# Kernel optimization log

Measured on AMD Instinct MI355X. Metric: run time of the kernel, lower is better.

The kernel has to match this reference:

```python
import jax, jax.numpy as jnp
import numpy as np
import math

B, S, D, H, E = 4, 4096, 256, 8, 262144
HD = D // H
ITER_NUM = 4
TEMP = 1.0
LN_EPS = 1e-12
N = B * S


def setup_inputs() -> dict:
    key = jax.random.key(0)
    ks = jax.random.split(key, 6)
    return {
        "hidden_states": jax.random.normal(ks[0], (B, S, D), dtype=jnp.float32),
        "attention_mask": jnp.zeros((B, S), dtype=jnp.float32),
        "src": jax.random.randint(ks[1], (E,), 0, N),
        "dst": jax.random.randint(ks[2], (E,), 0, N),
        "Wqkv": jax.random.normal(ks[3], (D, 3 * D), dtype=jnp.float32) * 0.02,
        "bqkv": jnp.zeros((3 * D,), dtype=jnp.float32),
        "Wo": jax.random.normal(ks[4], (D, D), dtype=jnp.float32) * 0.02,
        "bo": jnp.zeros((D,), dtype=jnp.float32),
        "gamma": jnp.ones((D,), dtype=jnp.float32),
        "beta": jnp.zeros((D,), dtype=jnp.float32),
    }


def _gn_attn(hidden_states, attention_mask, src, dst, Wqkv, bqkv, Wo, bo, gamma, beta):
    # qkv projection (node ordering is batch-major: node = b*S + s)
    qkv = hidden_states @ Wqkv + bqkv                      # [B,S,3D]
    q, k, v = jnp.split(qkv, 3, axis=-1)
    q = q / math.sqrt(HD)
    qn = q.reshape(N, H, HD)
    kn = k.reshape(N, H, HD)
    vn = v.reshape(N, H, HD)
    node_mask = (attention_mask >= 0).reshape(N)           # [N] bool

    # per-edge dot-product scores: u_dot_v('k','q') -> dot(k[src], q[dst])
    score = jnp.einsum("ehd,ehd->eh", kn[src], qn[dst])    # [E,H]
    edge_mask = node_mask[src] & node_mask[dst]
    score = jnp.where(edge_mask[:, None], score, jnp.float32(-10000.0))

    # edge softmax over incoming edges of each dst node (per head)
    mx = jax.ops.segment_max(score, dst, num_segments=N)   # [N,H]
    es = jnp.exp(score - mx[dst])
    den = jax.ops.segment_sum(es, dst, num_segments=N)     # [N,H]
    attn = es / den[dst]                                   # [E,H]

    # diffusion (heat-kernel / PPR-style) message passing
    h = math.exp(-TEMP) * vn                               # [N,H,HD]
    gather = h
    fact = 1.0
    for ki in range(1, ITER_NUM):
        msg = attn[:, :, None] * h[src]                    # [E,H,HD]
        h = jax.ops.segment_sum(msg, dst, num_segments=N)  # [N,H,HD]
        fact = fact * (TEMP / ki)
        gather = gather + fact * h

    attn_out = gather.reshape(B, S, D)

    # output projection + residual + LayerNorm
    y = attn_out @ Wo + bo + hidden_states
    mu = jnp.mean(y, axis=-1, keepdims=True)
    var = jnp.mean(jnp.square(y - mu), axis=-1, keepdims=True)
    return (y - mu) / jnp.sqrt(var + LN_EPS) * gamma + beta


def reference(hidden_states, attention_mask, src, dst, Wqkv, bqkv, Wo, bo, gamma, beta):
    return _gn_attn(hidden_states, attention_mask, src, dst, Wqkv, bqkv, Wo, bo, gamma, beta)
```

## Files before the change

kernel.cpp:

```cpp
#include <hip/hip_runtime.h>
#include <math.h>

#define NN 16384
#define DD 256
#define HH 8
#define EE 262144
#define D3 768
#define QSCALE 0.17677669529663687f
#define EXPN1 0.36787944117144233f
#define LN_EPS 1e-12f

typedef short bf16x8 __attribute__((ext_vector_type(8)));
typedef float f32x4 __attribute__((ext_vector_type(4)));
typedef float f32x2 __attribute__((ext_vector_type(2)));
typedef unsigned short u16;
typedef unsigned char u8;

__device__ __forceinline__ float bf_lo(unsigned u) { return __uint_as_float(u << 16); }
__device__ __forceinline__ float bf_hi(unsigned u) { return __uint_as_float(u & 0xffff0000u); }
__device__ __forceinline__ unsigned f2bf(float f) {
    unsigned b = __float_as_uint(f);
    return (b + 0x7fffu + ((b >> 16) & 1u)) >> 16;
}
__device__ __forceinline__ unsigned pack2bf(float lo, float hi) {
    return f2bf(lo) | (f2bf(hi) << 16);
}
__device__ __forceinline__ u8 f2fp8(float v) {
    return (u8)(__builtin_amdgcn_cvt_pk_fp8_f32(v, v, 0, false) & 0xff);
}

__global__ void prep_kernel(const float* __restrict__ hidden, unsigned* __restrict__ hidb,
                            const float* __restrict__ Wqkv, const float* __restrict__ bqkv,
                            u16* __restrict__ WtQ, float* __restrict__ biasq,
                            const float* __restrict__ Wo, const float* __restrict__ bo,
                            u16* __restrict__ WtO, float* __restrict__ biaso,
                            const int* __restrict__ dst, int* __restrict__ deg) {
    int b = blockIdx.x;
    if (b < 4096) {
        int gid = b * 256 + threadIdx.x;
        float4 v = *(const float4*)(hidden + (size_t)gid * 4);
        *(uint2*)(hidb + (size_t)gid * 2) = make_uint2(pack2bf(v.x, v.y), pack2bf(v.z, v.w));
    } else if (b < 4864) {
        int gid = (b - 4096) * 256 + threadIdx.x;
        int n = gid >> 8, k = gid & 255;
        float s = (n < DD) ? QSCALE : 1.0f;
        WtQ[(size_t)n * 256 + k] = (u16)f2bf(Wqkv[(size_t)k * D3 + n] * s);
        if (k == 0) biasq[n] = bqkv[n] * s;
    } else if (b < 5120) {
        int gid = (b - 4864) * 256 + threadIdx.x;
        int n = gid >> 8, k = gid & 255;
        WtO[(size_t)n * 256 + k] = (u16)f2bf(Wo[(size_t)k * DD + n]);
        if (k == 0) biaso[n] = bo[n];
    } else {
        int e = (b - 5120) * 256 + threadIdx.x;
        atomicAdd(&deg[dst[e]], 1);
    }
}

__global__ __launch_bounds__(256) void mfma_gemm1_kernel(
        const u16* __restrict__ Ab, const u16* __restrict__ Bt,
        const float* __restrict__ bias,
        u16* __restrict__ qb, u8* __restrict__ kb8,
        u8* __restrict__ h8, u16* __restrict__ gb) {
    __shared__ u16 As[128 * 40];
    __shared__ u16 Bs[128 * 40];
    const int tid = threadIdx.x;
    const int m0 = blockIdx.y * 128;
    const int n0 = blockIdx.x * 128;
    const int wave = tid >> 6, lane = tid & 63;
    const int wr = wave >> 1, wc = wave & 1;
    const int lm = lane & 15, quad = lane >> 4;

    f32x4 acc[4][4] = {};
    const int r0 = tid >> 2;
    const int c8 = (tid & 3) * 8;

    for (int k0 = 0; k0 < 256; k0 += 32) {
        #pragma unroll
        for (int s = 0; s < 2; ++s) {
            int r = r0 + s * 64;
            *(uint4*)&As[r * 40 + c8] = *(const uint4*)(Ab + (size_t)(m0 + r) * 256 + k0 + c8);
            *(uint4*)&Bs[r * 40 + c8] = *(const uint4*)(Bt + (size_t)(n0 + r) * 256 + k0 + c8);
        }
        __syncthreads();
        bf16x8 af[4], bfv[4];
        #pragma unroll
        for (int mi = 0; mi < 4; ++mi)
            af[mi] = *(const bf16x8*)&As[(wr * 64 + mi * 16 + lm) * 40 + quad * 8];
        #pragma unroll
        for (int ni = 0; ni < 4; ++ni)
            bfv[ni] = *(const bf16x8*)&Bs[(wc * 64 + ni * 16 + lm) * 40 + quad * 8];
        #pragma unroll
        for (int mi = 0; mi < 4; ++mi)
            #pragma unroll
            for (int ni = 0; ni < 4; ++ni)
                acc[mi][ni] = __builtin_amdgcn_mfma_f32_16x16x32_bf16(
                    af[mi], bfv[ni], acc[mi][ni], 0, 0, 0);
        __syncthreads();
    }

    const int type = n0 >> 8;
    const int cb = n0 & 255;
    #pragma unroll
    for (int mi = 0; mi < 4; ++mi) {
        #pragma unroll
        for (int j = 0; j < 4; ++j) {
            int m = m0 + wr * 64 + mi * 16 + quad * 4 + j;
            #pragma unroll
            for (int ni = 0; ni < 4; ++ni) {
                int nl = wc * 64 + ni * 16 + lm;
                float val = acc[mi][ni][j] + bias[n0 + nl];
                size_t off = (size_t)m * 256 + cb + nl;
                if (type == 0) qb[off] = (u16)f2bf(val);
                else if (type == 1) kb8[off] = f2fp8(val);
                else {
                    float hx = val * EXPN1;
                    h8[off] = f2fp8(hx);
                    gb[off] = (u16)f2bf(hx);
                }
            }
        }
    }
}

__global__ __launch_bounds__(1024) void scan_kernel(const int* __restrict__ deg,
                                                    int* __restrict__ offs,
                                                    int* __restrict__ cursor, int n) {
    __shared__ int part[1024];
    int t = threadIdx.x;
    int base = t * 16;
    int local[16];
    int s = 0;
    #pragma unroll
    for (int i = 0; i < 16; ++i) { local[i] = s; s += deg[base + i]; }
    part[t] = s;
    __syncthreads();
    for (int d = 1; d < 1024; d <<= 1) {
        int add = (t >= d) ? part[t - d] : 0;
        __syncthreads();
        part[t] += add;
        __syncthreads();
    }
    int excl = part[t] - s;
    #pragma unroll
    for (int i = 0; i < 16; ++i) {
        offs[base + i] = excl + local[i];
        cursor[base + i] = excl + local[i];
    }
    if (t == 1023) offs[n] = excl + s;
}

__global__ void scatter_kernel(const int* __restrict__ src, const int* __restrict__ dst,
                               int* __restrict__ cursor, int* __restrict__ srcs) {
    int e = blockIdx.x * 256 + threadIdx.x;
    int pos = atomicAdd(&cursor[dst[e]], 1);
    srcs[pos] = src[e];
}

__device__ __forceinline__ float edge_score(const unsigned qq[16], const u8* __restrict__ kb8,
                                            const float* __restrict__ amask,
                                            int s, int h, bool dvalid) {
    const uint4* kp = (const uint4*)(kb8 + (size_t)s * 256 + h * 32);
    uint4 k0 = kp[0], k1 = kp[1];
    unsigned kk[8] = {k0.x, k0.y, k0.z, k0.w, k1.x, k1.y, k1.z, k1.w};
    float acc = 0.0f;
    #pragma unroll
    for (int t = 0; t < 8; ++t) {
        f32x2 a = __builtin_amdgcn_cvt_pk_f32_fp8(kk[t], false);
        f32x2 b = __builtin_amdgcn_cvt_pk_f32_fp8(kk[t], true);
        acc += a.x * bf_lo(qq[2 * t]) + a.y * bf_hi(qq[2 * t]);
        acc += b.x * bf_lo(qq[2 * t + 1]) + b.y * bf_hi(qq[2 * t + 1]);
    }
    bool valid = dvalid && (amask[s] >= 0.0f);
    return valid ? acc : -10000.0f;
}

__global__ __launch_bounds__(256) void edge_softmax_kernel(
        const unsigned* __restrict__ qb, const u8* __restrict__ kb8,
        const int* __restrict__ offs, const int* __restrict__ srcs,
        const float* __restrict__ amask, float* __restrict__ attn) {
    const int wave = threadIdx.x >> 6, lane = threadIdx.x & 63;
    const int node = blockIdx.x * 4 + wave;
    const int h = lane & 7;
    const int eo = lane >> 3;
    const int beg = offs[node], end = offs[node + 1];
    const int cnt = end - beg;
    const uint4* qp = (const uint4*)(qb + (size_t)node * 128 + h * 16);
    uint4 q0 = qp[0], q1 = qp[1], q2 = qp[2], q3 = qp[3];
    unsigned qq[16] = {q0.x, q0.y, q0.z, q0.w, q1.x, q1.y, q1.z, q1.w,
                       q2.x, q2.y, q2.z, q2.w, q3.x, q3.y, q3.z, q3.w};
    const bool dvalid = amask[node] >= 0.0f;

    if (cnt <= 64) {
        float esb[8];
        float m = -1e30f;
        #pragma unroll
        for (int it = 0; it < 8; ++it) {
            int i = beg + it * 8 + eo;
            float sc = -1e30f;
            if (i < end) sc = edge_score(qq, kb8, amask, srcs[i], h, dvalid);
            esb[it] = sc;
            m = fmaxf(m, sc);
        }
        m = fmaxf(m, __shfl_xor(m, 8));
        m = fmaxf(m, __shfl_xor(m, 16));
        m = fmaxf(m, __shfl_xor(m, 32));
        float den = 0.0f;
        #pragma unroll
        for (int it = 0; it < 8; ++it) {
            int i = beg + it * 8 + eo;
            if (i < end) { float es = __expf(esb[it] - m); esb[it] = es; den += es; }
        }
        den += __shfl_xor(den, 8);
        den += __shfl_xor(den, 16);
        den += __shfl_xor(den, 32);
        float iv = (cnt > 0) ? 1.0f / den : 0.0f;
        #pragma unroll
        for (int it = 0; it < 8; ++it) {
            int i = beg + it * 8 + eo;
            if (i < end) attn[(size_t)i * 8 + h] = esb[it] * iv;
        }
    } else {
        float m = -1e30f;
        for (int i0 = beg; i0 < end; i0 += 8) {
            int i = i0 + eo;
            if (i < end) {
                float sc = edge_score(qq, kb8, amask, srcs[i], h, dvalid);
                attn[(size_t)i * 8 + h] = sc;
                m = fmaxf(m, sc);
            }
        }
        m = fmaxf(m, __shfl_xor(m, 8));
        m = fmaxf(m, __shfl_xor(m, 16));
        m = fmaxf(m, __shfl_xor(m, 32));
        float den = 0.0f;
        for (int i0 = beg; i0 < end; i0 += 8) {
            int i = i0 + eo;
            if (i < end) {
                float es = __expf(attn[(size_t)i * 8 + h] - m);
                attn[(size_t)i * 8 + h] = es;
                den += es;
            }
        }
        den += __shfl_xor(den, 8);
        den += __shfl_xor(den, 16);
        den += __shfl_xor(den, 32);
        float iv = 1.0f / den;
        for (int i0 = beg; i0 < end; i0 += 8) {
            int i = i0 + eo;
            if (i < end) attn[(size_t)i * 8 + h] *= iv;
        }
    }
}

__global__ void diffuse_kernel(const int* __restrict__ offs, const int* __restrict__ srcs,
                               const float* __restrict__ attn,
                               const unsigned* __restrict__ hcur, unsigned* __restrict__ hnext,
                               uint2* __restrict__ gb, float fact) {
    int gid = blockIdx.x * 256 + threadIdx.x;
    int node = gid >> 6;
    int j2 = gid & 63;
    int h = j2 >> 3;
    int beg = offs[node], end = offs[node + 1];
    float a0 = 0.0f, a1 = 0.0f, a2 = 0.0f, a3 = 0.0f;
    int i = beg;
    for (; i + 8 <= end; i += 8) {
        int sarr[8]; float aarr[8]; unsigned hv[8];
        #pragma unroll
        for (int t = 0; t < 8; ++t) {
            sarr[t] = srcs[i + t];
            aarr[t] = attn[(size_t)(i + t) * 8 + h];
        }
        #pragma unroll
        for (int t = 0; t < 8; ++t) hv[t] = hcur[(size_t)sarr[t] * 64 + j2];
        #pragma unroll
        for (int t = 0; t < 8; ++t) {
            float a = aarr[t];
            f32x2 lo = __builtin_amdgcn_cvt_pk_f32_fp8(hv[t], false);
            f32x2 hi = __builtin_amdgcn_cvt_pk_f32_fp8(hv[t], true);
            a0 += a * lo.x; a1 += a * lo.y;
            a2 += a * hi.x; a3 += a * hi.y;
        }
    }
    if (i < end) {
        int cnt = end - i;
        int sarr[8]; float aarr[8]; unsigned hv[8];
        #pragma unroll
        for (int t = 0; t < 8; ++t) if (t < cnt) {
            sarr[t] = srcs[i + t];
            aarr[t] = attn[(size_t)(i + t) * 8 + h];
        }
        #pragma unroll
        for (int t = 0; t < 8; ++t) if (t < cnt) hv[t] = hcur[(size_t)sarr[t] * 64 + j2];
        #pragma unroll
        for (int t = 0; t < 8; ++t) if (t < cnt) {
            float a = aarr[t];
            f32x2 lo = __builtin_amdgcn_cvt_pk_f32_fp8(hv[t], false);
            f32x2 hi = __builtin_amdgcn_cvt_pk_f32_fp8(hv[t], true);
            a0 += a * lo.x; a1 += a * lo.y;
            a2 += a * hi.x; a3 += a * hi.y;
        }
    }
    if (hnext) {
        int pk = __builtin_amdgcn_cvt_pk_fp8_f32(a0, a1, 0, false);
        pk = __builtin_amdgcn_cvt_pk_fp8_f32(a2, a3, pk, true);
        hnext[(size_t)node * 64 + j2] = (unsigned)pk;
    }
    uint2* gp = gb + (size_t)node * 64 + j2;
    uint2 g = *gp;
    float g0 = bf_lo(g.x) + fact * a0;
    float g1 = bf_hi(g.x) + fact * a1;
    float g2 = bf_lo(g.y) + fact * a2;
    float g3 = bf_hi(g.y) + fact * a3;
    *gp = make_uint2(pack2bf(g0, g1), pack2bf(g2, g3));
}

__global__ __launch_bounds__(256) void gemm2_ln_kernel(
        const u16* __restrict__ Ab, const u16* __restrict__ Bt,
        const float* __restrict__ bias, const float* __restrict__ resid,
        const float* __restrict__ gamma, const float* __restrict__ beta,
        float* __restrict__ out) {
    __shared__ u16 As[64 * 40];
    __shared__ u16 Bs[256 * 40];
    const int tid = threadIdx.x;
    const int m0 = blockIdx.x * 64;
    const int wave = tid >> 6, lane = tid & 63;
    const int lm = lane & 15, quad = lane >> 4;

    f32x4 acc[16] = {};
    for (int k0 = 0; k0 < 256; k0 += 32) {
        *(uint4*)&As[(tid >> 2) * 40 + (tid & 3) * 8] =
            *(const uint4*)(Ab + (size_t)(m0 + (tid >> 2)) * 256 + k0 + (tid & 3) * 8);
        {
            const uint4* srcp = (const uint4*)(Bt + (size_t)tid * 256 + k0);
            uint4* dstp = (uint4*)&Bs[tid * 40];
            dstp[0] = srcp[0]; dstp[1] = srcp[1]; dstp[2] = srcp[2]; dstp[3] = srcp[3];
        }
        __syncthreads();
        bf16x8 af = *(const bf16x8*)&As[(wave * 16 + lm) * 40 + quad * 8];
        #pragma unroll
        for (int ni = 0; ni < 16; ++ni) {
            bf16x8 bfv = *(const bf16x8*)&Bs[(ni * 16 + lm) * 40 + quad * 8];
            acc[ni] = __builtin_amdgcn_mfma_f32_16x16x32_bf16(af, bfv, acc[ni], 0, 0, 0);
        }
        __syncthreads();
    }

    const int mrow = m0 + wave * 16 + quad * 4;
    float ga[16], be[16];
    float rowsum[4] = {}, rowsq[4] = {};
    #pragma unroll
    for (int ni = 0; ni < 16; ++ni) {
        int col = ni * 16 + lm;
        float bia = bias[col];
        ga[ni] = gamma[col]; be[ni] = beta[col];
        #pragma unroll
        for (int j = 0; j < 4; ++j) {
            float val = acc[ni][j] + bia + resid[(size_t)(mrow + j) * 256 + col];
            acc[ni][j] = val;
            rowsum[j] += val;
            rowsq[j] += val * val;
        }
    }
    #pragma unroll
    for (int j = 0; j < 4; ++j) {
        #pragma unroll
        for (int msk = 1; msk <= 8; msk <<= 1) {
            rowsum[j] += __shfl_xor(rowsum[j], msk);
            rowsq[j] += __shfl_xor(rowsq[j], msk);
        }
    }
    float mu[4], rstd[4];
    #pragma unroll
    for (int j = 0; j < 4; ++j) {
        mu[j] = rowsum[j] * (1.0f / 256.0f);
        float var = rowsq[j] * (1.0f / 256.0f) - mu[j] * mu[j];
        rstd[j] = 1.0f / sqrtf(var + LN_EPS);
    }
    #pragma unroll
    for (int ni = 0; ni < 16; ++ni) {
        int col = ni * 16 + lm;
        #pragma unroll
        for (int j = 0; j < 4; ++j)
            out[(size_t)(mrow + j) * 256 + col] = (acc[ni][j] - mu[j]) * rstd[j] * ga[ni] + be[ni];
    }
}

extern "C" void kernel_launch(void* const* d_in, const int* in_sizes, int n_in,
                              void* d_out, int out_size, void* d_ws, size_t ws_size,
                              hipStream_t stream) {
    const float* hidden = (const float*)d_in[0];
    const float* amask  = (const float*)d_in[1];
    const int*   src    = (const int*)d_in[2];
    const int*   dst    = (const int*)d_in[3];
    const float* Wqkv   = (const float*)d_in[4];
    const float* bqkv   = (const float*)d_in[5];
    const float* Wo     = (const float*)d_in[6];
    const float* bo     = (const float*)d_in[7];
    const float* gamma  = (const float*)d_in[8];
    const float* beta   = (const float*)d_in[9];
    float* out = (float*)d_out;

    char* p = (char*)d_ws;
    u16*      hidb   = (u16*)p;      p += (size_t)NN * DD * 2;
    u16*      WtQ    = (u16*)p;      p += (size_t)D3 * DD * 2;
    u16*      WtO    = (u16*)p;      p += (size_t)DD * DD * 2;
    float*    biasq  = (float*)p;    p += (size_t)D3 * 4;
    float*    biaso  = (float*)p;    p += (size_t)DD * 4;
    u16*      qb     = (u16*)p;      p += (size_t)NN * DD * 2;
    u8*       kb8    = (u8*)p;       p += (size_t)NN * DD;
    u8*       h8A    = (u8*)p;       p += (size_t)NN * DD;
    u8*       h8B    = (u8*)p;       p += (size_t)NN * DD;
    u16*      gb     = (u16*)p;      p += (size_t)NN * DD * 2;
    float*    attn   = (float*)p;    p += (size_t)EE * HH * 4;
    int*      deg    = (int*)p;      p += (size_t)NN * 4;
    int*      offs   = (int*)p;      p += (size_t)(NN + 1) * 4;
    int*      cursor = (int*)p;      p += (size_t)NN * 4;
    int*      srcs   = (int*)p;      p += (size_t)EE * 4;

    hipMemsetAsync(deg, 0, (size_t)NN * 4, stream);
    prep_kernel<<<6144, 256, 0, stream>>>(hidden, (unsigned*)hidb,
                                          Wqkv, bqkv, WtQ, biasq,
                                          Wo, bo, WtO, biaso, dst, deg);

    scan_kernel<<<1, 1024, 0, stream>>>(deg, offs, cursor, NN);
    scatter_kernel<<<EE / 256, 256, 0, stream>>>(src, dst, cursor, srcs);

    mfma_gemm1_kernel<<<dim3(D3 / 128, NN / 128), 256, 0, stream>>>(
        hidb, WtQ, biasq, qb, kb8, h8A, gb);

    edge_softmax_kernel<<<NN / 4, 256, 0, stream>>>(
        (const unsigned*)qb, kb8, offs, srcs, amask, attn);

    diffuse_kernel<<<(NN * 64) / 256, 256, 0, stream>>>(
        offs, srcs, attn, (const unsigned*)h8A, (unsigned*)h8B, (uint2*)gb, 1.0f);
    diffuse_kernel<<<(NN * 64) / 256, 256, 0, stream>>>(
        offs, srcs, attn, (const unsigned*)h8B, (unsigned*)h8A, (uint2*)gb, 0.5f);
    diffuse_kernel<<<(NN * 64) / 256, 256, 0, stream>>>(
        offs, srcs, attn, (const unsigned*)h8A, nullptr, (uint2*)gb, 1.0f / 6.0f);

    gemm2_ln_kernel<<<NN / 64, 256, 0, stream>>>(
        gb, WtO, biaso, hidden, gamma, beta, out);
}
```

Before: 222.8 us.

## Fuse scatter into GEMM1 launch and first diffusion into edge softmax

```diff
diff --git a/kernel.cpp b/kernel.cpp
--- a/kernel.cpp
+++ b/kernel.cpp
@@ -57,16 +57,52 @@
     }
 }
 
-__global__ __launch_bounds__(256) void mfma_gemm1_kernel(
+__global__ __launch_bounds__(1024) void scan_kernel(const int* __restrict__ deg,
+                                                    int* __restrict__ offs,
+                                                    int* __restrict__ cursor, int n) {
+    __shared__ int part[1024];
+    int t = threadIdx.x;
+    int base = t * 16;
+    int local[16];
+    int s = 0;
+    #pragma unroll
+    for (int i = 0; i < 16; ++i) { local[i] = s; s += deg[base + i]; }
+    part[t] = s;
+    __syncthreads();
+    for (int d = 1; d < 1024; d <<= 1) {
+        int add = (t >= d) ? part[t - d] : 0;
+        __syncthreads();
+        part[t] += add;
+        __syncthreads();
+    }
+    int excl = part[t] - s;
+    #pragma unroll
+    for (int i = 0; i < 16; ++i) {
+        offs[base + i] = excl + local[i];
+        cursor[base + i] = excl + local[i];
+    }
+    if (t == 1023) offs[n] = excl + s;
+}
+
+__global__ __launch_bounds__(256) void gemm1_scatter_kernel(
         const u16* __restrict__ Ab, const u16* __restrict__ Bt,
         const float* __restrict__ bias,
         u16* __restrict__ qb, u8* __restrict__ kb8,
-        u8* __restrict__ h8, u16* __restrict__ gb) {
+        u8* __restrict__ h8, u16* __restrict__ gb,
+        const int* __restrict__ src, const int* __restrict__ dst,
+        int* __restrict__ cursor, int* __restrict__ srcs) {
     __shared__ u16 As[128 * 40];
     __shared__ u16 Bs[128 * 40];
+    if (blockIdx.x < 1024) {
+        int e = blockIdx.x * 256 + threadIdx.x;
+        int pos = atomicAdd(&cursor[dst[e]], 1);
+        srcs[pos] = src[e];
+        return;
+    }
+    const int bid = blockIdx.x - 1024;
     const int tid = threadIdx.x;
-    const int m0 = blockIdx.y * 128;
-    const int n0 = blockIdx.x * 128;
+    const int m0 = (bid / 6) * 128;
+    const int n0 = (bid % 6) * 128;
     const int wave = tid >> 6, lane = tid & 63;
     const int wr = wave >> 1, wc = wave & 1;
     const int lm = lane & 15, quad = lane >> 4;
@@ -123,40 +159,6 @@
     }
 }
 
-__global__ __launch_bounds__(1024) void scan_kernel(const int* __restrict__ deg,
-                                                    int* __restrict__ offs,
-                                                    int* __restrict__ cursor, int n) {
-    __shared__ int part[1024];
-    int t = threadIdx.x;
-    int base = t * 16;
-    int local[16];
-    int s = 0;
-    #pragma unroll
-    for (int i = 0; i < 16; ++i) { local[i] = s; s += deg[base + i]; }
-    part[t] = s;
-    __syncthreads();
-    for (int d = 1; d < 1024; d <<= 1) {
-        int add = (t >= d) ? part[t - d] : 0;
-        __syncthreads();
-        part[t] += add;
-        __syncthreads();
-    }
-    int excl = part[t] - s;
-    #pragma unroll
-    for (int i = 0; i < 16; ++i) {
-        offs[base + i] = excl + local[i];
-        cursor[base + i] = excl + local[i];
-    }
-    if (t == 1023) offs[n] = excl + s;
-}
-
-__global__ void scatter_kernel(const int* __restrict__ src, const int* __restrict__ dst,
-                               int* __restrict__ cursor, int* __restrict__ srcs) {
-    int e = blockIdx.x * 256 + threadIdx.x;
-    int pos = atomicAdd(&cursor[dst[e]], 1);
-    srcs[pos] = src[e];
-}
-
 __device__ __forceinline__ float edge_score(const unsigned qq[16], const u8* __restrict__ kb8,
                                             const float* __restrict__ amask,
                                             int s, int h, bool dvalid) {
@@ -175,30 +177,44 @@
     return valid ? acc : -10000.0f;
 }
 
-__global__ __launch_bounds__(256) void edge_softmax_kernel(
+__global__ __launch_bounds__(256) void softmax_diffuse1_kernel(
         const unsigned* __restrict__ qb, const u8* __restrict__ kb8,
         const int* __restrict__ offs, const int* __restrict__ srcs,
-        const float* __restrict__ amask, float* __restrict__ attn) {
+        const float* __restrict__ amask, float* __restrict__ attn,
+        const unsigned* __restrict__ hA, unsigned* __restrict__ hB,
+        uint2* __restrict__ gb) {
+    __shared__ int   s_src[4][64];
+    __shared__ float s_att[4][512];
     const int wave = threadIdx.x >> 6, lane = threadIdx.x & 63;
     const int node = blockIdx.x * 4 + wave;
     const int h = lane & 7;
     const int eo = lane >> 3;
     const int beg = offs[node], end = offs[node + 1];
     const int cnt = end - beg;
+    const int j2 = lane;
+    uint2 g = gb[(size_t)node * 64 + j2];
+
     const uint4* qp = (const uint4*)(qb + (size_t)node * 128 + h * 16);
     uint4 q0 = qp[0], q1 = qp[1], q2 = qp[2], q3 = qp[3];
     unsigned qq[16] = {q0.x, q0.y, q0.z, q0.w, q1.x, q1.y, q1.z, q1.w,
                        q2.x, q2.y, q2.z, q2.w, q3.x, q3.y, q3.z, q3.w};
     const bool dvalid = amask[node] >= 0.0f;
-
-    if (cnt <= 64) {
+    const bool fast = (cnt <= 64);
+
+    if (fast) {
+        int sarr[8];
+        #pragma unroll
+        for (int it = 0; it < 8; ++it) {
+            int i = beg + it * 8 + eo;
+            sarr[it] = (i < end) ? srcs[i] : 0;
+        }
         float esb[8];
         float m = -1e30f;
         #pragma unroll
         for (int it = 0; it < 8; ++it) {
             int i = beg + it * 8 + eo;
             float sc = -1e30f;
-            if (i < end) sc = edge_score(qq, kb8, amask, srcs[i], h, dvalid);
+            if (i < end) sc = edge_score(qq, kb8, amask, sarr[it], h, dvalid);
             esb[it] = sc;
             m = fmaxf(m, sc);
         }
@@ -218,7 +234,12 @@
         #pragma unroll
         for (int it = 0; it < 8; ++it) {
             int i = beg + it * 8 + eo;
-            if (i < end) attn[(size_t)i * 8 + h] = esb[it] * iv;
+            if (i < end) {
+                float a = esb[it] * iv;
+                attn[(size_t)i * 8 + h] = a;
+                s_att[wave][(it * 8 + eo) * 8 + h] = a;
+                if (h == 0) s_src[wave][it * 8 + eo] = sarr[it];
+            }
         }
     } else {
         float m = -1e30f;
@@ -251,6 +272,62 @@
             if (i < end) attn[(size_t)i * 8 + h] *= iv;
         }
     }
+    __syncthreads();
+
+    const int hh = j2 >> 3;
+    float a0 = 0.0f, a1 = 0.0f, a2 = 0.0f, a3 = 0.0f;
+    if (fast) {
+        for (int e0 = 0; e0 < cnt; e0 += 8) {
+            int sa[8]; float aa[8]; unsigned hv[8];
+            #pragma unroll
+            for (int t = 0; t < 8; ++t) {
+                bool ok = (e0 + t < cnt);
+                sa[t] = ok ? s_src[wave][e0 + t] : 0;
+                aa[t] = ok ? s_att[wave][(e0 + t) * 8 + hh] : 0.0f;
+            }
+            #pragma unroll
+            for (int t = 0; t < 8; ++t)
+                hv[t] = (e0 + t < cnt) ? hA[(size_t)sa[t] * 64 + j2] : 0u;
+            #pragma unroll
+            for (int t = 0; t < 8; ++t) {
+                float a = aa[t];
+                f32x2 lo = __builtin_amdgcn_cvt_pk_f32_fp8(hv[t], false);
+                f32x2 hi = __builtin_amdgcn_cvt_pk_f32_fp8(hv[t], true);
+                a0 += a * lo.x; a1 += a * lo.y;
+                a2 += a * hi.x; a3 += a * hi.y;
+            }
+        }
+    } else {
+        for (int i0 = beg; i0 < end; i0 += 8) {
+            int lim = end - i0;
+            int sa[8]; float aa[8]; unsigned hv[8];
+            #pragma unroll
+            for (int t = 0; t < 8; ++t) {
+                bool ok = (t < lim);
+                sa[t] = ok ? srcs[i0 + t] : 0;
+                aa[t] = ok ? attn[(size_t)(i0 + t) * 8 + hh] : 0.0f;
+            }
+            #pragma unroll
+            for (int t = 0; t < 8; ++t)
+                hv[t] = (t < lim) ? hA[(size_t)sa[t] * 64 + j2] : 0u;
+            #pragma unroll
+            for (int t = 0; t < 8; ++t) {
+                float a = aa[t];
+                f32x2 lo = __builtin_amdgcn_cvt_pk_f32_fp8(hv[t], false);
+                f32x2 hi = __builtin_amdgcn_cvt_pk_f32_fp8(hv[t], true);
+                a0 += a * lo.x; a1 += a * lo.y;
+                a2 += a * hi.x; a3 += a * hi.y;
+            }
+        }
+    }
+    int pk = __builtin_amdgcn_cvt_pk_fp8_f32(a0, a1, 0, false);
+    pk = __builtin_amdgcn_cvt_pk_fp8_f32(a2, a3, pk, true);
+    hB[(size_t)node * 64 + j2] = (unsigned)pk;
+    float g0 = bf_lo(g.x) + a0;
+    float g1 = bf_hi(g.x) + a1;
+    float g2 = bf_lo(g.y) + a2;
+    float g3 = bf_hi(g.y) + a3;
+    gb[(size_t)node * 64 + j2] = make_uint2(pack2bf(g0, g1), pack2bf(g2, g3));
 }
 
 __global__ void diffuse_kernel(const int* __restrict__ offs, const int* __restrict__ srcs,
@@ -262,17 +339,30 @@
     int j2 = gid & 63;
     int h = j2 >> 3;
     int beg = offs[node], end = offs[node + 1];
+    uint2* gp = gb + (size_t)node * 64 + j2;
+    uint2 g = *gp;
     float a0 = 0.0f, a1 = 0.0f, a2 = 0.0f, a3 = 0.0f;
-    int i = beg;
-    for (; i + 8 <= end; i += 8) {
-        int sarr[8]; float aarr[8]; unsigned hv[8];
+    int nfull = (end - beg) >> 3;
+    int sarr[8]; float aarr[8];
+    if (nfull > 0) {
         #pragma unroll
         for (int t = 0; t < 8; ++t) {
-            sarr[t] = srcs[i + t];
-            aarr[t] = attn[(size_t)(i + t) * 8 + h];
-        }
+            sarr[t] = srcs[beg + t];
+            aarr[t] = attn[(size_t)(beg + t) * 8 + h];
+        }
+    }
+    for (int c = 0; c < nfull; ++c) {
+        unsigned hv[8];
         #pragma unroll
         for (int t = 0; t < 8; ++t) hv[t] = hcur[(size_t)sarr[t] * 64 + j2];
+        int sn[8]; float an[8];
+        bool more = (c + 1 < nfull);
+        int nb = beg + (c + 1) * 8;
+        #pragma unroll
+        for (int t = 0; t < 8; ++t) {
+            sn[t] = more ? srcs[nb + t] : 0;
+            an[t] = more ? attn[(size_t)(nb + t) * 8 + h] : 0.0f;
+        }
         #pragma unroll
         for (int t = 0; t < 8; ++t) {
             float a = aarr[t];
@@ -281,20 +371,25 @@
             a0 += a * lo.x; a1 += a * lo.y;
             a2 += a * hi.x; a3 += a * hi.y;
         }
-    }
+        #pragma unroll
+        for (int t = 0; t < 8; ++t) { sarr[t] = sn[t]; aarr[t] = an[t]; }
+    }
+    int i = beg + nfull * 8;
     if (i < end) {
-        int cnt = end - i;
-        int sarr[8]; float aarr[8]; unsigned hv[8];
-        #pragma unroll
-        for (int t = 0; t < 8; ++t) if (t < cnt) {
-            sarr[t] = srcs[i + t];
-            aarr[t] = attn[(size_t)(i + t) * 8 + h];
-        }
-        #pragma unroll
-        for (int t = 0; t < 8; ++t) if (t < cnt) hv[t] = hcur[(size_t)sarr[t] * 64 + j2];
-        #pragma unroll
-        for (int t = 0; t < 8; ++t) if (t < cnt) {
-            float a = aarr[t];
+        int lim = end - i;
+        int sa[8]; float aa[8]; unsigned hv[8];
+        #pragma unroll
+        for (int t = 0; t < 8; ++t) {
+            bool ok = (t < lim);
+            sa[t] = ok ? srcs[i + t] : 0;
+            aa[t] = ok ? attn[(size_t)(i + t) * 8 + h] : 0.0f;
+        }
+        #pragma unroll
+        for (int t = 0; t < 8; ++t)
+            hv[t] = (t < lim) ? hcur[(size_t)sa[t] * 64 + j2] : 0u;
+        #pragma unroll
+        for (int t = 0; t < 8; ++t) {
+            float a = aa[t];
             f32x2 lo = __builtin_amdgcn_cvt_pk_f32_fp8(hv[t], false);
             f32x2 hi = __builtin_amdgcn_cvt_pk_f32_fp8(hv[t], true);
             a0 += a * lo.x; a1 += a * lo.y;
@@ -306,8 +401,6 @@
         pk = __builtin_amdgcn_cvt_pk_fp8_f32(a2, a3, pk, true);
         hnext[(size_t)node * 64 + j2] = (unsigned)pk;
     }
-    uint2* gp = gb + (size_t)node * 64 + j2;
-    uint2 g = *gp;
     float g0 = bf_lo(g.x) + fact * a0;
     float g1 = bf_hi(g.x) + fact * a1;
     float g2 = bf_lo(g.y) + fact * a2;
@@ -424,16 +517,14 @@
                                           Wo, bo, WtO, biaso, dst, deg);
 
     scan_kernel<<<1, 1024, 0, stream>>>(deg, offs, cursor, NN);
-    scatter_kernel<<<EE / 256, 256, 0, stream>>>(src, dst, cursor, srcs);
-
-    mfma_gemm1_kernel<<<dim3(D3 / 128, NN / 128), 256, 0, stream>>>(
-        hidb, WtQ, biasq, qb, kb8, h8A, gb);
-
-    edge_softmax_kernel<<<NN / 4, 256, 0, stream>>>(
-        (const unsigned*)qb, kb8, offs, srcs, amask, attn);
-
-    diffuse_kernel<<<(NN * 64) / 256, 256, 0, stream>>>(
-        offs, srcs, attn, (const unsigned*)h8A, (unsigned*)h8B, (uint2*)gb, 1.0f);
+
+    gemm1_scatter_kernel<<<1792, 256, 0, stream>>>(
+        hidb, WtQ, biasq, qb, kb8, h8A, gb, src, dst, cursor, srcs);
+
+    softmax_diffuse1_kernel<<<NN / 4, 256, 0, stream>>>(
+        (const unsigned*)qb, kb8, offs, srcs, amask, attn,
+        (const unsigned*)h8A, (unsigned*)h8B, (uint2*)gb);
+
     diffuse_kernel<<<(NN * 64) / 256, 256, 0, stream>>>(
         offs, srcs, attn, (const unsigned*)h8B, (unsigned*)h8A, (uint2*)gb, 0.5f);
     diffuse_kernel<<<(NN * 64) / 256, 256, 0, stream>>>(
```

New measurement: 224.8 us. No clear change (+0.9%).
